# Kernel optimization log

Measured on AMD Instinct MI355X. Metric: run time of the kernel, lower is better.

## Reference

```python
import jax, jax.numpy as jnp
import numpy as np
from jax import lax

K = 16  # knn_k


def _mlp(x, W1, b1, W2, b2):
    h = jax.nn.gelu(x @ W1 + b1, approximate=False)  # torch nn.GELU default = exact
    return h @ W2 + b2


def setup_inputs() -> dict:
    key = jax.random.key(0)
    ks = jax.random.split(key, 10)
    B, N, F, H = 8, 4096, 64, 128

    def xav(k, shape):
        fan_in = shape[0]
        return (jax.random.normal(k, shape, jnp.float32) / np.sqrt(fan_in)).astype(jnp.float32)

    return {
        "coords": jax.random.normal(ks[0], (B, N, 3), jnp.float32),
        "features": jax.random.normal(ks[1], (B, N, F), jnp.float32),
        "inv_W1": xav(ks[2], (6, H)), "inv_b1": jnp.zeros((H,), jnp.float32),
        "inv_W2": xav(ks[3], (H, H)), "inv_b2": jnp.zeros((H,), jnp.float32),
        "feat_W1": xav(ks[4], (F, H)), "feat_b1": jnp.zeros((H,), jnp.float32),
        "feat_W2": xav(ks[5], (H, H)), "feat_b2": jnp.zeros((H,), jnp.float32),
        "sh_W1": xav(ks[6], (2 * H, H)), "sh_b1": jnp.zeros((H,), jnp.float32),
        "sh_W2": xav(ks[7], (H, H)), "sh_b2": jnp.zeros((H,), jnp.float32),
        "g0_W": xav(ks[8], (H, 1)), "g0_b": jnp.zeros((1,), jnp.float32),
    }


def _local_geometry(coords):
    # coords: [B,N,3]
    B, N, _ = coords.shape
    k = min(K, N - 1)
    # squared pairwise distances (monotone in euclidean dist -> same kNN indices)
    sq = jnp.sum(coords * coords, axis=-1)                    # [B,N]
    dist2 = sq[:, :, None] + sq[:, None, :] - 2.0 * jnp.einsum("bnd,bmd->bnm", coords, coords)
    dist2 = lax.stop_gradient(dist2)
    eye = jnp.eye(N, dtype=bool)
    dist2 = jnp.where(eye[None], jnp.inf, dist2)
    _, idx = lax.top_k(-dist2, k)                             # smallest-k -> [B,N,k]
    neighbors = jax.vmap(lambda c, i: c[i])(coords, idx)      # [B,N,k,3]
    relative = neighbors - coords[:, :, None, :]              # [B,N,k,3]
    cov = jnp.einsum("bnki,bnkj->bnij", relative, relative) / float(k)  # [B,N,3,3]
    evals, evecs = jnp.linalg.eigh(cov)                       # ascending
    normals = evecs[..., 0]                                   # smallest-eigval eigenvector, [B,N,3]
    center = coords.mean(axis=1, keepdims=True)
    outward = coords - center
    orient = jnp.sign(jnp.sum(normals * outward, axis=-1, keepdims=True))
    orient = jnp.where(orient == 0, 1.0, orient)
    normals = normals * orient
    normals = normals / jnp.maximum(jnp.linalg.norm(normals, axis=-1, keepdims=True), 1e-6)
    radius = jnp.linalg.norm(relative, axis=-1).mean(axis=-1, keepdims=True)   # [B,N,1]
    centered_radius = jnp.linalg.norm(outward, axis=-1, keepdims=True)
    eig_sum = jnp.maximum(evals.sum(axis=-1, keepdims=True), 1e-6)
    dominance = evals[..., 2:3] / eig_sum
    invariants = jnp.concatenate([evals, radius, centered_radius, dominance], axis=-1)  # [B,N,6]
    return normals, invariants


def reference(coords, features, inv_W1, inv_b1, inv_W2, inv_b2,
              feat_W1, feat_b1, feat_W2, feat_b2,
              sh_W1, sh_b1, sh_W2, sh_b2, g0_W, g0_b):
    normals, invariants = _local_geometry(coords)
    inv_h = _mlp(invariants, inv_W1, inv_b1, inv_W2, inv_b2)
    feat_h = _mlp(features, feat_W1, feat_b1, feat_W2, feat_b2)
    hidden = _mlp(jnp.concatenate([inv_h, feat_h], axis=-1), sh_W1, sh_b1, sh_W2, sh_b2)
    scalar = hidden @ g0_W + g0_b                                   # grade 0, [B,N,1]
    plane = jnp.stack([normals[..., 0], normals[..., 1], -normals[..., 2],
                       -jnp.sum(coords * normals, axis=-1)], axis=-1)  # grade 1, [B,N,4]
    biv = jnp.concatenate([normals, jnp.zeros_like(normals)], axis=-1)  # grade 2, [B,N,6]
    point = jnp.concatenate([coords, jnp.ones(coords.shape[:-1] + (1,), coords.dtype)], axis=-1)  # grade 3 OPNS point
    zero4 = jnp.zeros(coords.shape[:-1] + (1,), coords.dtype)            # grade 4
    return jnp.concatenate([scalar, plane, biv, point, zero4], axis=-1)  # [B,N,16]
```

## Files before the change

kernel.cpp:

```cpp
#include <hip/hip_runtime.h>
#include <hip/hip_bf16.h>

#define BB 8
#define NN 4096
#define FF 64
#define HH 128
#define KNN 16

typedef __attribute__((ext_vector_type(8))) short bf16x8;
typedef __attribute__((ext_vector_type(4))) short bf16x4;
typedef __attribute__((ext_vector_type(4))) float f32x4;

#define OFF_iW2 0
#define OFF_fW1 16384
#define OFF_fW2 24576
#define OFF_sW1 40960
#define OFF_sW2 73728
#define HI_SZ   90112

__device__ __forceinline__ float sq3(float x, float y, float z) {
    return fmaf(z, z, fmaf(y, y, __fmul_rn(x, x)));
}
__device__ __forceinline__ float dist2f(float px, float py, float pz, float psq, float4 cc) {
    float t = fmaf(pz, cc.z, fmaf(py, cc.y, __fmul_rn(px, cc.x)));
    return __fsub_rn(__fadd_rn(psq, cc.w), __fmul_rn(2.0f, t));
}

__device__ __forceinline__ short f2bf(float x) {
    unsigned u = __float_as_uint(x);
    u += 0x7fffu + ((u >> 16) & 1u);
    return (short)(u >> 16);
}
__device__ __forceinline__ float bf2f(short s) {
    return __uint_as_float(((unsigned)(unsigned short)s) << 16);
}

extern "C" __global__ __launch_bounds__(256)
void k_prep(const float* __restrict__ coords, float4* __restrict__ coords4, float* __restrict__ center,
            const float* __restrict__ iW2, const float* __restrict__ fW1,
            const float* __restrict__ fW2, const float* __restrict__ sW1,
            const float* __restrict__ sW2, short* __restrict__ wbf) {
    const int bx = blockIdx.x, tid = threadIdx.x;
    __shared__ float rx[256], ry[256], rz[256];
    if (bx < 8) {
        const int b = bx;
        float sx = 0.f, sy = 0.f, sz = 0.f;
        for (int n = tid; n < NN; n += 256) {
            const float* c = coords + (size_t)(b * NN + n) * 3;
            float x = c[0], y = c[1], z = c[2];
            coords4[b * NN + n] = make_float4(x, y, z, sq3(x, y, z));
            sx += x; sy += y; sz += z;
        }
        rx[tid] = sx; ry[tid] = sy; rz[tid] = sz;
        __syncthreads();
        for (int s = 128; s > 0; s >>= 1) {
            if (tid < s) { rx[tid] += rx[tid + s]; ry[tid] += ry[tid + s]; rz[tid] += rz[tid + s]; }
            __syncthreads();
        }
        if (tid == 0) {
            center[b * 4 + 0] = rx[0] * (1.0f / NN);
            center[b * 4 + 1] = ry[0] * (1.0f / NN);
            center[b * 4 + 2] = rz[0] * (1.0f / NN);
        }
    } else {
        const int wb = bx - 8;
        const int w = wb >> 4;
        const int xb = wb & 15;
        const float* W; int K; int off;
        if (w == 0)      { W = iW2; K = 128; off = OFF_iW2; }
        else if (w == 1) { W = fW1; K = 64;  off = OFF_fW1; }
        else if (w == 2) { W = fW2; K = 128; off = OFF_fW2; }
        else if (w == 3) { W = sW1; K = 256; off = OFF_sW1; }
        else             { W = sW2; K = 128; off = OFF_sW2; }
        short* hi = wbf + off;
        short* lo = wbf + HI_SZ + off;
        const int total = K * 128;
        for (int e = xb * 256 + tid; e < total; e += 4096) {
            int j = e & 7, lane = (e >> 3) & 63, ct = (e >> 9) & 7, kb = e >> 12;
            int k = kb * 32 + (lane >> 4) * 8 + j;
            int n = ct * 16 + (lane & 15);
            float v = W[k * 128 + n];
            short h = f2bf(v);
            float r = v - bf2f(h);
            hi[e] = h; lo[e] = f2bf(r);
        }
    }
}

#define JROT(app, aqq, apq, arp, arq, vp0, vp1, vp2, vq0, vq1, vq2) { \
    float tau_ = (aqq - app) / (2.0f * apq); \
    float tt_ = copysignf(1.0f, tau_) / (fabsf(tau_) + sqrtf(1.0f + tau_ * tau_)); \
    if (apq == 0.0f) tt_ = 0.0f; \
    float cc_ = 1.0f / sqrtf(1.0f + tt_ * tt_); \
    float ss_ = tt_ * cc_; \
    float app_n = cc_*cc_*app - 2.0f*cc_*ss_*apq + ss_*ss_*aqq; \
    float aqq_n = ss_*ss_*app + 2.0f*cc_*ss_*apq + cc_*cc_*aqq; \
    float apq_n = cc_*ss_*(app - aqq) + (cc_*cc_ - ss_*ss_)*apq; \
    float arp_n = cc_*arp - ss_*arq; \
    float arq_n = ss_*arp + cc_*arq; \
    app = app_n; aqq = aqq_n; apq = apq_n; arp = arp_n; arq = arq_n; \
    float t0_ = cc_*vp0 - ss_*vq0, t1_ = cc_*vp1 - ss_*vq1, t2_ = cc_*vp2 - ss_*vq2; \
    vq0 = ss_*vp0 + cc_*vq0; vq1 = ss_*vp1 + cc_*vq1; vq2 = ss_*vp2 + cc_*vq2; \
    vp0 = t0_; vp1 = t1_; vp2 = t2_; }

#define SWAPF(a, b) { float sw_ = a; a = b; b = sw_; }

__device__ __forceinline__ void ce(float& a, float& b) {
    float mn = fminf(a, b);
    b = fmaxf(a, b);
    a = mn;
}

__device__ __forceinline__ void sort16(float (&d)[16]) {
    ce(d[0],d[1]); ce(d[2],d[3]); ce(d[0],d[2]); ce(d[1],d[3]); ce(d[1],d[2]);
    ce(d[4],d[5]); ce(d[6],d[7]); ce(d[4],d[6]); ce(d[5],d[7]); ce(d[5],d[6]);
    ce(d[0],d[4]); ce(d[2],d[6]); ce(d[2],d[4]);
    ce(d[1],d[5]); ce(d[3],d[7]); ce(d[3],d[5]);
    ce(d[1],d[2]); ce(d[3],d[4]); ce(d[5],d[6]);
    ce(d[8],d[9]); ce(d[10],d[11]); ce(d[8],d[10]); ce(d[9],d[11]); ce(d[9],d[10]);
    ce(d[12],d[13]); ce(d[14],d[15]); ce(d[12],d[14]); ce(d[13],d[15]); ce(d[13],d[14]);
    ce(d[8],d[12]); ce(d[10],d[14]); ce(d[10],d[12]);
    ce(d[9],d[13]); ce(d[11],d[15]); ce(d[11],d[13]);
    ce(d[9],d[10]); ce(d[11],d[12]); ce(d[13],d[14]);
    ce(d[0],d[8]); ce(d[4],d[12]); ce(d[4],d[8]);
    ce(d[2],d[10]); ce(d[6],d[14]); ce(d[6],d[10]);
    ce(d[2],d[4]); ce(d[6],d[8]); ce(d[10],d[12]);
    ce(d[1],d[9]); ce(d[5],d[13]); ce(d[5],d[9]);
    ce(d[3],d[11]); ce(d[7],d[15]); ce(d[7],d[11]);
    ce(d[3],d[5]); ce(d[7],d[9]); ce(d[11],d[13]);
    ce(d[1],d[2]); ce(d[3],d[4]); ce(d[5],d[6]); ce(d[7],d[8]);
    ce(d[9],d[10]); ce(d[11],d[12]); ce(d[13],d[14]);
}

__device__ __forceinline__ void merge16(float (&dk)[16], float (&d)[16]) {
#pragma unroll
    for (int i = 0; i < 8; i++) {
        float a  = fminf(dk[i], d[15 - i]);
        float b2 = fminf(dk[15 - i], d[i]);
        d[i] = a; d[15 - i] = b2;
    }
#pragma unroll
    for (int j = 8; j > 0; j >>= 1)
#pragma unroll
        for (int i = 0; i < 16; i++) {
            int l = i ^ j;
            if (l > i) ce(d[i], d[l]);
        }
#pragma unroll
    for (int i = 0; i < 16; i++) dk[i] = d[i];
}

__device__ __forceinline__ void sort16i(int (&d)[16]) {
#pragma unroll
    for (int k = 2; k <= 16; k <<= 1) {
#pragma unroll
        for (int j = k >> 1; j > 0; j >>= 1) {
#pragma unroll
            for (int i = 0; i < 16; i++) {
                int l = i ^ j;
                if (l > i) {
                    int a = d[i], bq = d[l];
                    int mn = a < bq ? a : bq;
                    int mx = a < bq ? bq : a;
                    if ((i & k) == 0) { d[i] = mn; d[l] = mx; }
                    else              { d[i] = mx; d[l] = mn; }
                }
            }
        }
    }
}

extern "C" __global__ __launch_bounds__(512, 8)
void k_knn(const float4* __restrict__ coords4, const float* __restrict__ center,
           float* __restrict__ inv8g, float* __restrict__ out) {
    const int blk = blockIdx.x;
    const int b = blk >> 7;
    const int chunk = blk & 127;
    const int tid = threadIdx.x;
    const int h = tid & 15;
    const int pid = tid >> 4;
    const int n = chunk * 32 + pid;
    const float4* __restrict__ C = coords4 + b * NN;

    __shared__ __align__(16) float4 tile[1024];
    __shared__ unsigned short slist[512];
    __shared__ unsigned short tlist[256];
    __shared__ int cnt_s[32];
    __shared__ int cnt_t[32];

    if (tid < 32) { cnt_s[tid] = 0; cnt_t[tid] = 0; }

    float4 me = C[n];
    const float px = me.x, py = me.y, pz = me.z, psq = me.w;
    const float INF = __builtin_inff();

    float dk[KNN];
#pragma unroll
    for (int i = 0; i < KNN; i++) dk[i] = INF;

    for (int r = 0; r < 4; r++) {
        __syncthreads();
        tile[tid] = C[r * 1024 + tid];
        tile[tid + 512] = C[r * 1024 + tid + 512];
        __syncthreads();
#pragma unroll
        for (int bt = 0; bt < 4; bt++) {
            float d[16];
#pragma unroll
            for (int i = 0; i < 16; i++) {
                float4 cc = tile[bt * 256 + i * 16 + h];
                float dd = dist2f(px, py, pz, psq, cc);
                int g = r * 1024 + bt * 256 + i * 16 + h;
                d[i] = (g == n) ? INF : dd;
            }
            sort16(d);
            merge16(dk, d);
        }
    }

#pragma unroll
    for (int m = 1; m <= 8; m <<= 1) {
        float o[16];
#pragma unroll
        for (int i = 0; i < KNN; i++) o[i] = __shfl_xor(dk[i], m);
        merge16(dk, o);
    }
    const float d15 = dk[15];

    for (int r = 0; r < 4; r++) {
        __syncthreads();
        tile[tid] = C[r * 1024 + tid];
        tile[tid + 512] = C[r * 1024 + tid + 512];
        __syncthreads();
#pragma unroll 4
        for (int j16 = 0; j16 < 64; j16++) {
            float4 cc = tile[j16 * 16 + h];
            float d = dist2f(px, py, pz, psq, cc);
            int g = r * 1024 + j16 * 16 + h;
            if (g != n && d <= d15) {
                if (d < d15) {
                    int pos = atomicAdd(&cnt_s[pid], 1);
                    if (pos < 16) slist[pid * 16 + pos] = (unsigned short)g;
                } else {
                    int pos = atomicAdd(&cnt_t[pid], 1);
                    if (pos < 8) tlist[pid * 8 + pos] = (unsigned short)g;
                }
            }
        }
    }
    __syncthreads();

    if (tid < 32) {
        const int np = chunk * 32 + tid;
        float4 pme = C[np];
        int ns = cnt_s[tid]; ns = ns > 15 ? 15 : ns;
        int ids[16];
#pragma unroll
        for (int j = 0; j < 16; j++) {
            int tj = j - ns; tj = tj < 0 ? 0 : (tj > 7 ? 7 : tj);
            int sid = (int)slist[tid * 16 + j];
            int tie = (int)tlist[tid * 8 + tj];
            ids[j] = (j < ns) ? sid : tie;
        }
        sort16i(ids);

        float cxx = 0.f, cxy = 0.f, cxz = 0.f, cyy = 0.f, cyz = 0.f, czz = 0.f, radsum = 0.f;
#pragma unroll
        for (int j = 0; j < KNN; j++) {
            float4 cc = C[ids[j]];
            float rx = __fsub_rn(cc.x, pme.x), ry = __fsub_rn(cc.y, pme.y), rz = __fsub_rn(cc.z, pme.z);
            cxx = __fadd_rn(cxx, __fmul_rn(rx, rx));
            cxy = __fadd_rn(cxy, __fmul_rn(rx, ry));
            cxz = __fadd_rn(cxz, __fmul_rn(rx, rz));
            cyy = __fadd_rn(cyy, __fmul_rn(ry, ry));
            cyz = __fadd_rn(cyz, __fmul_rn(ry, rz));
            czz = __fadd_rn(czz, __fmul_rn(rz, rz));
            float rr = __fadd_rn(__fadd_rn(__fmul_rn(rx, rx), __fmul_rn(ry, ry)), __fmul_rn(rz, rz));
            radsum = __fadd_rn(radsum, sqrtf(rr));
        }
        const float inv_k = 1.0f / KNN;
        float a00 = cxx * inv_k, a01 = cxy * inv_k, a02 = cxz * inv_k;
        float a11 = cyy * inv_k, a12 = cyz * inv_k, a22 = czz * inv_k;

        float V00 = 1.f, V01 = 0.f, V02 = 0.f;
        float V10 = 0.f, V11 = 1.f, V12 = 0.f;
        float V20 = 0.f, V21 = 0.f, V22 = 1.f;
        for (int sweep = 0; sweep < 6; sweep++) {
            JROT(a00, a11, a01, a02, a12, V00, V10, V20, V01, V11, V21);
            JROT(a00, a22, a02, a01, a12, V00, V10, V20, V02, V12, V22);
            JROT(a11, a22, a12, a01, a02, V01, V11, V21, V02, V12, V22);
        }
        float e0 = a00, e1 = a11, e2 = a22;
        float x0 = V00, y0 = V10, z0 = V20;
        float x1 = V01, y1 = V11, z1 = V21;
        float x2 = V02, y2 = V12, z2 = V22;
        if (e0 > e1) { SWAPF(e0, e1); SWAPF(x0, x1); SWAPF(y0, y1); SWAPF(z0, z1); }
        if (e1 > e2) { SWAPF(e1, e2); SWAPF(x1, x2); SWAPF(y1, y2); SWAPF(z1, z2); }
        if (e0 > e1) { SWAPF(e0, e1); SWAPF(x0, x1); SWAPF(y0, y1); SWAPF(z0, z1); }

        float cx = center[b * 4 + 0], cy = center[b * 4 + 1], cz = center[b * 4 + 2];
        float ox = __fsub_rn(pme.x, cx), oy = __fsub_rn(pme.y, cy), oz = __fsub_rn(pme.z, cz);
        float dt = __fadd_rn(__fadd_rn(__fmul_rn(x0, ox), __fmul_rn(y0, oy)), __fmul_rn(z0, oz));
        float sgn = (dt >= 0.0f) ? 1.0f : -1.0f;
        x0 *= sgn; y0 *= sgn; z0 *= sgn;
        float nrm = sqrtf(__fadd_rn(__fadd_rn(__fmul_rn(x0, x0), __fmul_rn(y0, y0)), __fmul_rn(z0, z0)));
        float den = fmaxf(nrm, 1e-6f);
        x0 = x0 / den; y0 = y0 / den; z0 = z0 / den;

        float radius = radsum * inv_k;
        float crad = sqrtf(__fadd_rn(__fadd_rn(__fmul_rn(ox, ox), __fmul_rn(oy, oy)), __fmul_rn(oz, oz)));
        float esum = fmaxf(__fadd_rn(__fadd_rn(e0, e1), e2), 1e-6f);
        float dom = e2 / esum;

        float* ip = inv8g + (size_t)(b * NN + np) * 8;
        ip[0] = e0; ip[1] = e1; ip[2] = e2; ip[3] = radius; ip[4] = crad; ip[5] = dom;
        ip[6] = 0.f; ip[7] = 0.f;

        float pd = __fadd_rn(__fadd_rn(__fmul_rn(pme.x, x0), __fmul_rn(pme.y, y0)), __fmul_rn(pme.z, z0));
        float4* o = (float4*)(out + (size_t)(b * NN + np) * 16);
        o[0] = make_float4(0.0f, x0, y0, -z0);
        o[1] = make_float4(-pd, x0, y0, z0);
        o[2] = make_float4(0.0f, 0.0f, 0.0f, pme.x);
        o[3] = make_float4(pme.y, pme.z, 1.0f, 0.0f);
    }
}

__device__ __forceinline__ float gelu_exact(float x) {
    return 0.5f * x * (1.0f + erff(x * 0.70710678118654752440f));
}

template <int KB, bool INIT>
__device__ __forceinline__ void gemm_mfma(const short* Ab, const short* __restrict__ whi,
                                          const short* __restrict__ wlo,
                                          const float* __restrict__ bias,
                                          int wid, int lane, f32x4 acc[2]) {
    const int m16 = lane & 15, quad = lane >> 4;
    if (INIT) {
        float b0 = bias[wid * 16 + m16];
        acc[0] = (f32x4){b0, b0, b0, b0};
        acc[1] = acc[0];
    }
#pragma unroll 1
    for (int kb = 0; kb < KB; kb++) {
        bf16x8 a0 = *(const bf16x8*)(Ab + m16 * 136 + kb * 32 + quad * 8);
        bf16x8 a1 = *(const bf16x8*)(Ab + (m16 + 16) * 136 + kb * 32 + quad * 8);
        const int off = ((kb * 8 + wid) * 64 + lane) * 8;
        bf16x8 bh = *(const bf16x8*)(whi + off);
        bf16x8 bl = *(const bf16x8*)(wlo + off);
        acc[0] = __builtin_amdgcn_mfma_f32_16x16x32_bf16(a0, bh, acc[0], 0, 0, 0);
        acc[0] = __builtin_amdgcn_mfma_f32_16x16x32_bf16(a0, bl, acc[0], 0, 0, 0);
        acc[1] = __builtin_amdgcn_mfma_f32_16x16x32_bf16(a1, bh, acc[1], 0, 0, 0);
        acc[1] = __builtin_amdgcn_mfma_f32_16x16x32_bf16(a1, bl, acc[1], 0, 0, 0);
    }
}

__device__ __forceinline__ void acc_to_bf(short* dst, f32x4 acc[2], int wid, int lane, bool dogelu) {
    const int m16 = lane & 15, quad = lane >> 4;
#pragma unroll
    for (int mt = 0; mt < 2; mt++)
#pragma unroll
        for (int i = 0; i < 4; i++) {
            float v = acc[mt][i];
            if (dogelu) v = gelu_exact(v);
            dst[(mt * 16 + quad * 4 + i) * 136 + wid * 16 + m16] = f2bf(v);
        }
}

extern "C" __global__ __launch_bounds__(512, 8)
void k_mlp(const float* __restrict__ features, const short* __restrict__ wbf,
           const float* __restrict__ iW1, const float* __restrict__ ib1,
           const float* __restrict__ ib2,
           const float* __restrict__ fb1, const float* __restrict__ fb2,
           const float* __restrict__ sb1, const float* __restrict__ sb2,
           const float* __restrict__ gW, const float* __restrict__ gb,
           const float* __restrict__ inv8g, float* __restrict__ out) {
    const int blk = blockIdx.x;
    const int b = blk >> 7;
    const int chunk = blk & 127;
    const int tid = threadIdx.x;

    __shared__ __align__(16) float inv8[256];
    __shared__ float sc[32];
    __shared__ __align__(16) short Abf[32 * 136];
    __shared__ __align__(16) short FHbf[32 * 136];

    const int wid = tid >> 6, lane = tid & 63;
    const short* w_iW2h = wbf + OFF_iW2; const short* w_iW2l = wbf + HI_SZ + OFF_iW2;
    const short* w_fW1h = wbf + OFF_fW1; const short* w_fW1l = wbf + HI_SZ + OFF_fW1;
    const short* w_fW2h = wbf + OFF_fW2; const short* w_fW2l = wbf + HI_SZ + OFF_fW2;
    const short* w_sW1h = wbf + OFF_sW1; const short* w_sW1l = wbf + HI_SZ + OFF_sW1;
    const short* w_sW2h = wbf + OFF_sW2; const short* w_sW2l = wbf + HI_SZ + OFF_sW2;
    f32x4 acc[2];

    if (tid < 256) inv8[tid] = inv8g[(size_t)(b * NN + chunk * 32) * 8 + tid];
    if (tid < 32) sc[tid] = gb[0];
    {
        int row = tid >> 4, c4 = (tid & 15) * 4;
        const float* s = features + (size_t)(b * NN + chunk * 32 + row) * FF + c4;
        float4 v = *(const float4*)s;
        bf16x4 pk;
        pk[0] = f2bf(v.x); pk[1] = f2bf(v.y); pk[2] = f2bf(v.z); pk[3] = f2bf(v.w);
        *(bf16x4*)(Abf + row * 136 + c4) = pk;
    }
    __syncthreads();

    gemm_mfma<2, true>(Abf, w_fW1h, w_fW1l, fb1, wid, lane, acc);
    __syncthreads();
    acc_to_bf(Abf, acc, wid, lane, true);
    __syncthreads();

    gemm_mfma<4, true>(Abf, w_fW2h, w_fW2l, fb2, wid, lane, acc);
    __syncthreads();
    acc_to_bf(FHbf, acc, wid, lane, false);

    {
        const int cg = tid & 31, pg = tid >> 5;
        const int c0 = cg * 4, p0 = pg * 2;
        float4 bb = *(const float4*)(ib1 + c0);
        float a2[2][4];
#pragma unroll
        for (int i = 0; i < 2; i++) { a2[i][0] = bb.x; a2[i][1] = bb.y; a2[i][2] = bb.z; a2[i][3] = bb.w; }
#pragma unroll
        for (int k = 0; k < 6; k++) {
            float4 w = *(const float4*)(iW1 + k * HH + c0);
#pragma unroll
            for (int i = 0; i < 2; i++) {
                float a = inv8[(p0 + i) * 8 + k];
                a2[i][0] = fmaf(a, w.x, a2[i][0]);
                a2[i][1] = fmaf(a, w.y, a2[i][1]);
                a2[i][2] = fmaf(a, w.z, a2[i][2]);
                a2[i][3] = fmaf(a, w.w, a2[i][3]);
            }
        }
#pragma unroll
        for (int i = 0; i < 2; i++) {
            bf16x4 pk;
            pk[0] = f2bf(gelu_exact(a2[i][0])); pk[1] = f2bf(gelu_exact(a2[i][1]));
            pk[2] = f2bf(gelu_exact(a2[i][2])); pk[3] = f2bf(gelu_exact(a2[i][3]));
            *(bf16x4*)(Abf + (p0 + i) * 136 + c0) = pk;
        }
    }
    __syncthreads();

    gemm_mfma<4, true>(Abf, w_iW2h, w_iW2l, ib2, wid, lane, acc);
    __syncthreads();
    acc_to_bf(Abf, acc, wid, lane, false);
    __syncthreads();

    gemm_mfma<4, true>(Abf, w_sW1h, w_sW1l, sb1, wid, lane, acc);
    gemm_mfma<4, false>(FHbf, w_sW1h + 16384, w_sW1l + 16384, nullptr, wid, lane, acc);
    __syncthreads();
    acc_to_bf(Abf, acc, wid, lane, true);
    __syncthreads();

    gemm_mfma<4, true>(Abf, w_sW2h, w_sW2l, sb2, wid, lane, acc);
    {
        const int m16 = lane & 15, quad = lane >> 4;
        float g = gW[wid * 16 + m16];
#pragma unroll
        for (int mt = 0; mt < 2; mt++)
#pragma unroll
            for (int i = 0; i < 4; i++)
                atomicAdd(&sc[mt * 16 + quad * 4 + i], acc[mt][i] * g);
    }
    __syncthreads();
    if (tid < 32) out[(size_t)(b * NN + chunk * 32 + tid) * 16] = sc[tid];
}

extern "C" void kernel_launch(void* const* d_in, const int* in_sizes, int n_in,
                              void* d_out, int out_size, void* d_ws, size_t ws_size,
                              hipStream_t stream) {
    const float* coords   = (const float*)d_in[0];
    const float* features = (const float*)d_in[1];
    const float* iW1 = (const float*)d_in[2],  * ib1 = (const float*)d_in[3];
    const float* iW2 = (const float*)d_in[4],  * ib2 = (const float*)d_in[5];
    const float* fW1 = (const float*)d_in[6],  * fb1 = (const float*)d_in[7];
    const float* fW2 = (const float*)d_in[8],  * fb2 = (const float*)d_in[9];
    const float* sW1 = (const float*)d_in[10], * sb1 = (const float*)d_in[11];
    const float* sW2 = (const float*)d_in[12], * sb2 = (const float*)d_in[13];
    const float* gW  = (const float*)d_in[14], * gb  = (const float*)d_in[15];
    float* out = (float*)d_out;

    char* ws = (char*)d_ws;
    float4* coords4 = (float4*)ws;
    float* center   = (float*)(ws + 524288);
    short* wbf      = (short*)(ws + 524416);
    float* inv8g    = (float*)(ws + 884864);

    hipLaunchKernelGGL(k_prep, dim3(88), dim3(256), 0, stream,
                       coords, coords4, center, iW2, fW1, fW2, sW1, sW2, wbf);
    hipLaunchKernelGGL(k_knn, dim3(1024), dim3(512), 0, stream, coords4, center, inv8g, out);
    hipLaunchKernelGGL(k_mlp, dim3(1024), dim3(512), 0, stream, features, wbf,
                       iW1, ib1, ib2, fb1, fb2, sb1, sb2, gW, gb, inv8g, out);
}
```

Baseline: 263.8 us.

## Use separate LDS buffers in MLP kernel to drop intermediate barriers

The MLP kernel now gives each intermediate activation its own shared-memory buffer (FAbf, IAbf, Hbf, FHbf) instead of reusing one. This lets it remove about half of the __syncthreads calls between GEMM stages and overlap the invariant-MLP first layer with the feature GEMM. merge16 also writes its result in place, dropping a 16-element register copy. The cost is more LDS per block, which may lower occupancy under the launch bounds of 512 threads and 8 blocks.

```diff
diff --git a/kernel.cpp b/kernel.cpp
--- a/kernel.cpp
+++ b/kernel.cpp
@@ -132,22 +132,20 @@
     ce(d[9],d[10]); ce(d[11],d[12]); ce(d[13],d[14]);
 }
 
-__device__ __forceinline__ void merge16(float (&dk)[16], float (&d)[16]) {
+__device__ __forceinline__ void merge16(float (&dk)[16], const float (&d)[16]) {
 #pragma unroll
     for (int i = 0; i < 8; i++) {
         float a  = fminf(dk[i], d[15 - i]);
         float b2 = fminf(dk[15 - i], d[i]);
-        d[i] = a; d[15 - i] = b2;
+        dk[i] = a; dk[15 - i] = b2;
     }
 #pragma unroll
     for (int j = 8; j > 0; j >>= 1)
 #pragma unroll
         for (int i = 0; i < 16; i++) {
             int l = i ^ j;
-            if (l > i) ce(d[i], d[l]);
-        }
-#pragma unroll
-    for (int i = 0; i < 16; i++) dk[i] = d[i];
+            if (l > i) ce(dk[i], dk[l]);
+        }
 }
 
 __device__ __forceinline__ void sort16i(int (&d)[16]) {
@@ -381,7 +379,9 @@
 
     __shared__ __align__(16) float inv8[256];
     __shared__ float sc[32];
-    __shared__ __align__(16) short Abf[32 * 136];
+    __shared__ __align__(16) short FAbf[32 * 136];
+    __shared__ __align__(16) short IAbf[32 * 136];
+    __shared__ __align__(16) short Hbf[32 * 136];
     __shared__ __align__(16) short FHbf[32 * 136];
 
     const int wid = tid >> 6, lane = tid & 63;
@@ -400,19 +400,11 @@
         float4 v = *(const float4*)s;
         bf16x4 pk;
         pk[0] = f2bf(v.x); pk[1] = f2bf(v.y); pk[2] = f2bf(v.z); pk[3] = f2bf(v.w);
-        *(bf16x4*)(Abf + row * 136 + c4) = pk;
-    }
-    __syncthreads();
-
-    gemm_mfma<2, true>(Abf, w_fW1h, w_fW1l, fb1, wid, lane, acc);
-    __syncthreads();
-    acc_to_bf(Abf, acc, wid, lane, true);
-    __syncthreads();
-
-    gemm_mfma<4, true>(Abf, w_fW2h, w_fW2l, fb2, wid, lane, acc);
-    __syncthreads();
-    acc_to_bf(FHbf, acc, wid, lane, false);
-
+        *(bf16x4*)(FAbf + row * 136 + c4) = pk;
+    }
+    __syncthreads();
+
+    gemm_mfma<2, true>(FAbf, w_fW1h, w_fW1l, fb1, wid, lane, acc);
     {
         const int cg = tid & 31, pg = tid >> 5;
         const int c0 = cg * 4, p0 = pg * 2;
@@ -437,23 +429,26 @@
             bf16x4 pk;
             pk[0] = f2bf(gelu_exact(a2[i][0])); pk[1] = f2bf(gelu_exact(a2[i][1]));
             pk[2] = f2bf(gelu_exact(a2[i][2])); pk[3] = f2bf(gelu_exact(a2[i][3]));
-            *(bf16x4*)(Abf + (p0 + i) * 136 + c0) = pk;
-        }
-    }
-    __syncthreads();
-
-    gemm_mfma<4, true>(Abf, w_iW2h, w_iW2l, ib2, wid, lane, acc);
-    __syncthreads();
-    acc_to_bf(Abf, acc, wid, lane, false);
-    __syncthreads();
-
-    gemm_mfma<4, true>(Abf, w_sW1h, w_sW1l, sb1, wid, lane, acc);
+            *(bf16x4*)(IAbf + (p0 + i) * 136 + c0) = pk;
+        }
+    }
+    acc_to_bf(Hbf, acc, wid, lane, true);
+    __syncthreads();
+
+    gemm_mfma<4, true>(Hbf, w_fW2h, w_fW2l, fb2, wid, lane, acc);
+    acc_to_bf(FHbf, acc, wid, lane, false);
+    __syncthreads();
+
+    gemm_mfma<4, true>(IAbf, w_iW2h, w_iW2l, ib2, wid, lane, acc);
+    acc_to_bf(Hbf, acc, wid, lane, false);
+    __syncthreads();
+
+    gemm_mfma<4, true>(Hbf, w_sW1h, w_sW1l, sb1, wid, lane, acc);
     gemm_mfma<4, false>(FHbf, w_sW1h + 16384, w_sW1l + 16384, nullptr, wid, lane, acc);
-    __syncthreads();
-    acc_to_bf(Abf, acc, wid, lane, true);
-    __syncthreads();
-
-    gemm_mfma<4, true>(Abf, w_sW2h, w_sW2l, sb2, wid, lane, acc);
+    acc_to_bf(IAbf, acc, wid, lane, true);
+    __syncthreads();
+
+    gemm_mfma<4, true>(IAbf, w_sW2h, w_sW2l, sb2, wid, lane, acc);
     {
         const int m16 = lane & 15, quad = lane >> 4;
         float g = gW[wid * 16 + m16];
```

Result: no change. 266.5 us (+1.0%).
